# Kernel optimization log

Hardware: AMD Instinct MI355X
Metric: run time of the kernel (lower is better)

Reference implementation:

```python
import jax, jax.numpy as jnp
import numpy as np


def setup_inputs() -> dict:
    key = jax.random.key(0)
    ks = jax.random.split(key, 10)
    B, L, Din, Dout = 64, 512, 256, 256
    s = 0.05
    inp = jax.random.normal(ks[0], (B, L, Din), jnp.float32)
    ci = jax.random.randint(ks[1], (B, L), 0, L)
    # valid coref indices: ci[:, i] must be in [0, i] (refers to an already-produced state)
    ci = ci % (jnp.arange(L) + 1)[None, :]
    p = lambda k, sh: jax.random.normal(k, sh, jnp.float32) * s
    return {
        "inp": inp,
        "last_coref_idx": ci,
        "Wr": p(ks[2], (Din, Dout)), "br": jnp.zeros((Dout,), jnp.float32),
        "Ur": p(ks[3], (Dout, Dout)),
        "Wz": p(ks[4], (Din, Dout)), "bz": jnp.zeros((Dout,), jnp.float32),
        "Uz": p(ks[5], (Dout, Dout)),
        "Wh": p(ks[6], (Din, Dout)), "bh": jnp.zeros((Dout,), jnp.float32),
        "Uh": p(ks[7], (Dout, Dout)),
        "k1": p(ks[8], (Din, 1)),
        "k2": p(ks[9], (Din, 1)),
    }


def reference(inp, last_coref_idx, Wr, br, Ur, Wz, bz, Uz, Wh, bh, Uh, k1, k2):
    B, L, Din = inp.shape
    Dout = Wr.shape[1]
    split = Dout // 2
    bidx = jnp.arange(B)

    def step(carry, xs):
        h_last, hist = carry            # h_last [B,Dout], hist [L,B,Dout]
        x, c, i = xs                    # x [B,Din], c [B] int, i scalar step index
        # coref = state_history[c-1][b] if c > 0 else zeros
        coref = hist[jnp.clip(c - 1, 0), bidx]
        coref = jnp.where((c > 0)[:, None], coref, jnp.zeros_like(coref))
        # attention between h_last-half and coref-half
        e = jnp.concatenate([x @ k1, x @ k2], axis=1)      # [B,2]
        a = jax.nn.softmax(e, axis=1)[:, 0:1]              # [B,1]
        mt = jnp.concatenate([a * h_last[:, :split], (1.0 - a) * coref[:, split:]], axis=1)
        r = jax.nn.sigmoid(x @ Wr + br + mt @ Ur)
        z = jax.nn.sigmoid(x @ Wz + bz + mt @ Uz)
        h_ = jnp.tanh(x @ Wh + bh + r * (mt @ Uh))
        h = (1.0 - z) * mt + z * h_
        hist = jax.lax.dynamic_update_index_in_dim(hist, h, i, 0)
        return (h, hist), h

    h0 = jnp.zeros((B, Dout), inp.dtype)
    hist0 = jnp.zeros((L, B, Dout), inp.dtype)
    xs = (jnp.swapaxes(inp, 0, 1), jnp.swapaxes(last_coref_idx, 0, 1), jnp.arange(L))
    _, ys = jax.lax.scan(step, (h0, hist0), xs)            # ys [L,B,Dout]
    return jnp.swapaxes(ys, 0, 1)                          # [B,L,Dout]
```

## Files before the change

### kernel.cpp

```cpp
#include <hip/hip_runtime.h>
#include <stdint.h>
#include <stddef.h>

typedef _Float16 half_t;
typedef _Float16 half2_t __attribute__((ext_vector_type(2)));
typedef _Float16 half8_t __attribute__((ext_vector_type(8)));
typedef float    floatx4 __attribute__((ext_vector_type(4)));
typedef uint32_t u32x4   __attribute__((ext_vector_type(4)));
typedef int      intx4   __attribute__((ext_vector_type(4)));

#define SEQ_L 512
#define NBATCH 64
#define DIM 256
#define NTOT (NBATCH * SEQ_L)

__device__ __forceinline__ int dot4i8(uint32_t a, uint32_t b, int c) {
#if defined(__has_builtin)
#if __has_builtin(__builtin_amdgcn_sdot4)
  return __builtin_amdgcn_sdot4((int)a, (int)b, c, false);
#else
  int s = c;
  s += (int)(int8_t)(a)       * (int)(int8_t)(b);
  s += (int)(int8_t)(a >> 8)  * (int)(int8_t)(b >> 8);
  s += (int)(int8_t)(a >> 16) * (int)(int8_t)(b >> 16);
  s += (int)(int8_t)(a >> 24) * (int)(int8_t)(b >> 24);
  return s;
#endif
#else
  int s = c;
  s += (int)(int8_t)(a)       * (int)(int8_t)(b);
  s += (int)(int8_t)(a >> 8)  * (int)(int8_t)(b >> 8);
  s += (int)(int8_t)(a >> 16) * (int)(int8_t)(b >> 16);
  s += (int)(int8_t)(a >> 24) * (int)(int8_t)(b >> 24);
  return s;
#endif
}

__device__ __forceinline__ float sigmoidf_fast(float x) {
  return 1.0f / (1.0f + __expf(-x));
}
__device__ __forceinline__ float tanhf_fast(float x) {
  float e = __expf(2.0f * x);
  return 1.0f - 2.0f / (e + 1.0f);
}

__global__ void conv_w_kernel(const float* __restrict__ Wr,
                              const float* __restrict__ Wz,
                              const float* __restrict__ Wh,
                              half_t* __restrict__ Wt) {
  int n = blockIdx.x;
  int k = threadIdx.x;
  const float* W = (n < 256) ? Wr : ((n < 512) ? Wz : Wh);
  int j = n & 255;
  Wt[(size_t)n * DIM + k] = (half_t)W[(size_t)k * DIM + j];
}

__global__ __launch_bounds__(256) void attn_a_kernel(const float* __restrict__ inp,
                                                     const float* __restrict__ k1,
                                                     const float* __restrict__ k2,
                                                     float* __restrict__ a_arr) {
  int row  = blockIdx.x * 4 + (threadIdx.x >> 6);
  int lane = threadIdx.x & 63;
  const float4* x4 = (const float4*)(inp + (size_t)row * DIM);
  float4 xv  = x4[lane];
  float4 k1v = ((const float4*)k1)[lane];
  float4 k2v = ((const float4*)k2)[lane];
  float e1 = xv.x * k1v.x + xv.y * k1v.y + xv.z * k1v.z + xv.w * k1v.w;
  float e2 = xv.x * k2v.x + xv.y * k2v.y + xv.z * k2v.z + xv.w * k2v.w;
#pragma unroll
  for (int off = 32; off >= 1; off >>= 1) {
    e1 += __shfl_xor(e1, off);
    e2 += __shfl_xor(e2, off);
  }
  if (lane == 0) a_arr[row] = 1.0f / (1.0f + __expf(e2 - e1));
}

__global__ __launch_bounds__(256) void uscale_kernel(const float* __restrict__ Ur,
                                                     const float* __restrict__ Uz,
                                                     const float* __restrict__ Uh,
                                                     float* __restrict__ su) {
  const int g = blockIdx.x;
  const int j = threadIdx.x;
  const float* U = (g == 0) ? Ur : ((g == 1) ? Uz : Uh);
  float m = 0.0f;
  for (int k = 0; k < DIM; ++k) m = fmaxf(m, fabsf(U[(size_t)k * DIM + j]));
  su[g * DIM + j] = fmaxf(m, 1e-30f) * (1.0f / 127.0f);
}

__global__ __launch_bounds__(256) void upack_kernel(const float* __restrict__ Ur,
                                                    const float* __restrict__ Uz,
                                                    const float* __restrict__ Uh,
                                                    const float* __restrict__ su,
                                                    uint32_t* __restrict__ Ui8) {
  const int g = blockIdx.x;
  const int j = threadIdx.x;
  const float* U = (g == 0) ? Ur : ((g == 1) ? Uz : Uh);
  const float r = 1.0f / su[g * DIM + j];
  for (int q = 0; q < 64; ++q) {
    uint32_t w = 0;
#pragma unroll
    for (int t = 0; t < 4; ++t) {
      float v = U[(size_t)(q * 4 + t) * DIM + j] * r;
      int mi = __float2int_rn(v);
      mi = mi < -127 ? -127 : (mi > 127 ? 127 : mi);
      w |= ((uint32_t)(mi & 0xFF)) << (8 * t);
    }
    Ui8[((size_t)g * 64 + q) * DIM + j] = w;
  }
}

__global__ __launch_bounds__(256) void gemm_p_kernel(const float* __restrict__ X,
                                                     const half_t* __restrict__ Wt,
                                                     half_t* __restrict__ P) {
  __shared__ __align__(16) half_t As[128][32];
  __shared__ __align__(16) half_t Bs[128][32];
  const int tid  = threadIdx.x;
  const int bm   = blockIdx.x * 128;
  const int bn   = blockIdx.y * 128;
  const int lane = tid & 63;
  const int wave = tid >> 6;
  const int wm   = (wave >> 1) * 64;
  const int wn   = (wave & 1) * 64;
  const int quad = lane >> 4;
  const int l15  = lane & 15;
  const int r0   = tid >> 2;
  const int kc   = (tid & 3) * 8;

  floatx4 acc[4][4] = {};

  for (int k0 = 0; k0 < DIM; k0 += 32) {
#pragma unroll
    for (int hh = 0; hh < 2; ++hh) {
      int r = r0 + hh * 64;
      const float* asrc = X + (size_t)(bm + r) * DIM + k0 + kc;
      float4 f0 = *(const float4*)(asrc);
      float4 f1 = *(const float4*)(asrc + 4);
      half8_t av;
      av[0] = (half_t)f0.x; av[1] = (half_t)f0.y; av[2] = (half_t)f0.z; av[3] = (half_t)f0.w;
      av[4] = (half_t)f1.x; av[5] = (half_t)f1.y; av[6] = (half_t)f1.z; av[7] = (half_t)f1.w;
      *(half8_t*)(&As[r][kc]) = av;
      *(half8_t*)(&Bs[r][kc]) = *(const half8_t*)(Wt + (size_t)(bn + r) * DIM + k0 + kc);
    }
    __syncthreads();
    half8_t af[4], bf[4];
#pragma unroll
    for (int mi = 0; mi < 4; ++mi)
      af[mi] = *(const half8_t*)(&As[wm + mi * 16 + l15][quad * 8]);
#pragma unroll
    for (int ni = 0; ni < 4; ++ni)
      bf[ni] = *(const half8_t*)(&Bs[wn + ni * 16 + l15][quad * 8]);
#pragma unroll
    for (int mi = 0; mi < 4; ++mi)
#pragma unroll
      for (int ni = 0; ni < 4; ++ni)
        acc[mi][ni] = __builtin_amdgcn_mfma_f32_16x16x32_f16(af[mi], bf[ni], acc[mi][ni], 0, 0, 0);
    __syncthreads();
  }
#pragma unroll
  for (int mi = 0; mi < 4; ++mi)
#pragma unroll
    for (int ni = 0; ni < 4; ++ni) {
      int col = bn + wn + ni * 16 + l15;
#pragma unroll
      for (int rr = 0; rr < 4; ++rr) {
        int row = bm + wm + mi * 16 + quad * 4 + rr;
        P[(size_t)row * 768 + col] = (half_t)acc[mi][ni][rr];
      }
    }
}

__global__ __launch_bounds__(256, 1) void recur_kernel(
    const half_t* __restrict__ P,
    const float* __restrict__ a_arr,
    const int* __restrict__ cidx,
    const uint32_t* __restrict__ Ui8,
    const float* __restrict__ su,
    const float* __restrict__ br, const float* __restrict__ bz, const float* __restrict__ bh,
    float* __restrict__ out) {
  const int j = threadIdx.x;

  __shared__ __align__(16) half_t   hist[SEQ_L][128];
  __shared__ __align__(16) uint32_t mtb[2][64];

  u32x4 ur8[16], uz8[16], uh8[16];
#pragma unroll
  for (int c8 = 0; c8 < 16; ++c8) {
#pragma unroll
    for (int t = 0; t < 4; ++t) {
      const int quad = c8 * 4 + t;
      ur8[c8][t] = Ui8[((size_t)0 * 64 + quad) * DIM + j];
      uz8[c8][t] = Ui8[((size_t)1 * 64 + quad) * DIM + j];
      uh8[c8][t] = Ui8[((size_t)2 * 64 + quad) * DIM + j];
    }
  }

  const float scr = su[0 * DIM + j] * (1.0f / 127.0f);
  const float scz = su[1 * DIM + j] * (1.0f / 127.0f);
  const float sch = su[2 * DIM + j] * (1.0f / 127.0f);
  const float brj = br[j], bzj = bz[j], bhj = bh[j];

  if (j < 64) mtb[0][j] = 0u;

  float mtj = 0.0f;
  const int base = blockIdx.x * SEQ_L;

  const half_t* prow0 = P + (size_t)base * 768;
  float pr_c = (float)prow0[j];
  float pz_c = (float)prow0[DIM + j];
  float ph_c = (float)prow0[2 * DIM + j];
  float a_n = a_arr[base + 1];
  int   c_n = cidx[base + 1];

  __syncthreads();

  for (int i = 0; i < SEQ_L; ++i) {
#pragma unroll
    for (int g8 = 0; g8 < 2; ++g8) {
      asm volatile("" : "+v"(ur8[g8*8+0]), "+v"(ur8[g8*8+1]), "+v"(ur8[g8*8+2]), "+v"(ur8[g8*8+3]),
                         "+v"(ur8[g8*8+4]), "+v"(ur8[g8*8+5]), "+v"(ur8[g8*8+6]), "+v"(ur8[g8*8+7]));
      asm volatile("" : "+v"(uz8[g8*8+0]), "+v"(uz8[g8*8+1]), "+v"(uz8[g8*8+2]), "+v"(uz8[g8*8+3]),
                         "+v"(uz8[g8*8+4]), "+v"(uz8[g8*8+5]), "+v"(uz8[g8*8+6]), "+v"(uz8[g8*8+7]));
      asm volatile("" : "+v"(uh8[g8*8+0]), "+v"(uh8[g8*8+1]), "+v"(uh8[g8*8+2]), "+v"(uh8[g8*8+3]),
                         "+v"(uh8[g8*8+4]), "+v"(uh8[g8*8+5]), "+v"(uh8[g8*8+6]), "+v"(uh8[g8*8+7]));
    }

    const int  cp    = c_n - 1;
    const bool use_h = (cp == i);
    float corefv = 0.0f;
    if (j >= 128) {
      if (c_n > 0 && !use_h) corefv = (float)hist[cp][j - 128];
    }

    const int ip1 = (i + 1 < SEQ_L) ? (i + 1) : i;
    const half_t* prow = P + (size_t)(base + ip1) * 768;
    float pr_x = (float)prow[j];
    float pz_x = (float)prow[DIM + j];
    float ph_x = (float)prow[2 * DIM + j];
    const int ip2 = (i + 2 < SEQ_L) ? (i + 2) : (SEQ_L - 1);
    const float a_x = a_arr[base + ip2];
    const int   c_x = cidx[base + ip2];

    int ar = 0, az = 0, ah = 0;
    const u32x4* mq = (const u32x4*)(&mtb[i & 1][0]);
#pragma unroll
    for (int c8 = 0; c8 < 16; ++c8) {
      u32x4 m4 = mq[c8];
      ar = dot4i8(m4.x, ur8[c8][0], ar);
      az = dot4i8(m4.x, uz8[c8][0], az);
      ah = dot4i8(m4.x, uh8[c8][0], ah);
      ar = dot4i8(m4.y, ur8[c8][1], ar);
      az = dot4i8(m4.y, uz8[c8][1], az);
      ah = dot4i8(m4.y, uh8[c8][1], ah);
      ar = dot4i8(m4.z, ur8[c8][2], ar);
      az = dot4i8(m4.z, uz8[c8][2], az);
      ah = dot4i8(m4.z, uh8[c8][2], ah);
      ar = dot4i8(m4.w, ur8[c8][3], ar);
      az = dot4i8(m4.w, uz8[c8][3], az);
      ah = dot4i8(m4.w, uh8[c8][3], ah);
    }

    const float fr = (float)ar * scr;
    const float fz = (float)az * scz;
    const float fh = (float)ah * sch;
    const float rg = sigmoidf_fast(pr_c + brj + fr);
    const float zg = sigmoidf_fast(pz_c + bzj + fz);
    const float hb = tanhf_fast(ph_c + bhj + rg * fh);
    const float h  = (1.0f - zg) * mtj + zg * hb;

    out[(size_t)(base + i) * DIM + j] = h;
    if (j >= 128) hist[i][j - 128] = (half_t)h;

    float mtn;
    if (j < 128) {
      mtn = a_n * h;
    } else {
      const float coref = (c_n > 0) ? (use_h ? h : corefv) : 0.0f;
      mtn = (1.0f - a_n) * coref;
    }
    mtj = mtn;

    int mi = __float2int_rn(mtn * 127.0f);
    mi = mi < -127 ? -127 : (mi > 127 ? 127 : mi);
    unsigned v0 = (unsigned)mi & 0xFFu;
    unsigned o1 = (unsigned)__shfl_xor((int)v0, 1) & 0xFFu;
    unsigned pp = (j & 1) ? (o1 | (v0 << 8)) : (v0 | (o1 << 8));
    unsigned o2 = (unsigned)__shfl_xor((int)pp, 2);
    unsigned qd = (j & 2) ? ((o2 & 0xFFFFu) | (pp << 16))
                          : ((pp & 0xFFFFu) | (o2 << 16));
    if ((j & 3) == 0) mtb[(i + 1) & 1][j >> 2] = qd;

    pr_c = pr_x; pz_c = pz_x; ph_c = ph_x;
    a_n = a_x;   c_n = c_x;

    __syncthreads();
  }
}

extern "C" void kernel_launch(void* const* d_in, const int* in_sizes, int n_in,
                              void* d_out, int out_size, void* d_ws, size_t ws_size,
                              hipStream_t stream) {
  const float* inp = (const float*)d_in[0];
  const int*   ci  = (const int*)d_in[1];
  const float* Wr  = (const float*)d_in[2];
  const float* br  = (const float*)d_in[3];
  const float* Ur  = (const float*)d_in[4];
  const float* Wz  = (const float*)d_in[5];
  const float* bz  = (const float*)d_in[6];
  const float* Uz  = (const float*)d_in[7];
  const float* Wh  = (const float*)d_in[8];
  const float* bh  = (const float*)d_in[9];
  const float* Uh  = (const float*)d_in[10];
  const float* k1  = (const float*)d_in[11];
  const float* k2  = (const float*)d_in[12];
  float* out = (float*)d_out;

  char* ws = (char*)d_ws;
  half_t*   Wt    = (half_t*)ws;
  half_t*   P     = (half_t*)(ws + 393216);
  float*    a_arr = (float*)(ws + 393216 + 50331648);
  float*    su    = (float*)(ws + 50855936);
  uint32_t* Ui8   = (uint32_t*)(ws + 50859008);

  conv_w_kernel<<<dim3(768), dim3(256), 0, stream>>>(Wr, Wz, Wh, Wt);
  attn_a_kernel<<<dim3(NTOT / 4), dim3(256), 0, stream>>>(inp, k1, k2, a_arr);
  uscale_kernel<<<dim3(3), dim3(256), 0, stream>>>(Ur, Uz, Uh, su);
  upack_kernel<<<dim3(3), dim3(256), 0, stream>>>(Ur, Uz, Uh, su, Ui8);
  gemm_p_kernel<<<dim3(NTOT / 128, 6), dim3(256), 0, stream>>>(inp, Wt, P);
  recur_kernel<<<dim3(NBATCH), dim3(256), 0, stream>>>(P, a_arr, ci, Ui8, su,
                                                       br, bz, bh, out);
}
```

Before: 665.1 us.

## Stream int8 recurrent weights from cache each step instead of holding in registers

```diff
diff --git a/kernel.cpp b/kernel.cpp
--- a/kernel.cpp
+++ b/kernel.cpp
@@ -91,7 +91,7 @@
                                                     const float* __restrict__ Uz,
                                                     const float* __restrict__ Uh,
                                                     const float* __restrict__ su,
-                                                    uint32_t* __restrict__ Ui8) {
+                                                    uint32_t* __restrict__ Ust) {
   const int g = blockIdx.x;
   const int j = threadIdx.x;
   const float* U = (g == 0) ? Ur : ((g == 1) ? Uz : Uh);
@@ -105,7 +105,8 @@
       mi = mi < -127 ? -127 : (mi > 127 ? 127 : mi);
       w |= ((uint32_t)(mi & 0xFF)) << (8 * t);
     }
-    Ui8[((size_t)g * 64 + q) * DIM + j] = w;
+    const int c = g * 16 + (q >> 2);
+    Ust[((size_t)c * 256 + j) * 4 + (q & 3)] = w;
   }
 }
 
@@ -173,7 +174,7 @@
     const half_t* __restrict__ P,
     const float* __restrict__ a_arr,
     const int* __restrict__ cidx,
-    const uint32_t* __restrict__ Ui8,
+    const uint32_t* __restrict__ Ust,
     const float* __restrict__ su,
     const float* __restrict__ br, const float* __restrict__ bz, const float* __restrict__ bh,
     float* __restrict__ out) {
@@ -182,22 +183,12 @@
   __shared__ __align__(16) half_t   hist[SEQ_L][128];
   __shared__ __align__(16) uint32_t mtb[2][64];
 
-  u32x4 ur8[16], uz8[16], uh8[16];
-#pragma unroll
-  for (int c8 = 0; c8 < 16; ++c8) {
-#pragma unroll
-    for (int t = 0; t < 4; ++t) {
-      const int quad = c8 * 4 + t;
-      ur8[c8][t] = Ui8[((size_t)0 * 64 + quad) * DIM + j];
-      uz8[c8][t] = Ui8[((size_t)1 * 64 + quad) * DIM + j];
-      uh8[c8][t] = Ui8[((size_t)2 * 64 + quad) * DIM + j];
-    }
-  }
-
   const float scr = su[0 * DIM + j] * (1.0f / 127.0f);
   const float scz = su[1 * DIM + j] * (1.0f / 127.0f);
   const float sch = su[2 * DIM + j] * (1.0f / 127.0f);
   const float brj = br[j], bzj = bz[j], bhj = bh[j];
+
+  const u32x4* upv = (const u32x4*)Ust;
 
   if (j < 64) mtb[0][j] = 0u;
 
@@ -214,15 +205,7 @@
   __syncthreads();
 
   for (int i = 0; i < SEQ_L; ++i) {
-#pragma unroll
-    for (int g8 = 0; g8 < 2; ++g8) {
-      asm volatile("" : "+v"(ur8[g8*8+0]), "+v"(ur8[g8*8+1]), "+v"(ur8[g8*8+2]), "+v"(ur8[g8*8+3]),
-                         "+v"(ur8[g8*8+4]), "+v"(ur8[g8*8+5]), "+v"(ur8[g8*8+6]), "+v"(ur8[g8*8+7]));
-      asm volatile("" : "+v"(uz8[g8*8+0]), "+v"(uz8[g8*8+1]), "+v"(uz8[g8*8+2]), "+v"(uz8[g8*8+3]),
-                         "+v"(uz8[g8*8+4]), "+v"(uz8[g8*8+5]), "+v"(uz8[g8*8+6]), "+v"(uz8[g8*8+7]));
-      asm volatile("" : "+v"(uh8[g8*8+0]), "+v"(uh8[g8*8+1]), "+v"(uh8[g8*8+2]), "+v"(uh8[g8*8+3]),
-                         "+v"(uh8[g8*8+4]), "+v"(uh8[g8*8+5]), "+v"(uh8[g8*8+6]), "+v"(uh8[g8*8+7]));
-    }
+    asm volatile("" : "+v"(upv));
 
     const int  cp    = c_n - 1;
     const bool use_h = (cp == i);
@@ -243,20 +226,23 @@
     int ar = 0, az = 0, ah = 0;
     const u32x4* mq = (const u32x4*)(&mtb[i & 1][0]);
 #pragma unroll
-    for (int c8 = 0; c8 < 16; ++c8) {
-      u32x4 m4 = mq[c8];
-      ar = dot4i8(m4.x, ur8[c8][0], ar);
-      az = dot4i8(m4.x, uz8[c8][0], az);
-      ah = dot4i8(m4.x, uh8[c8][0], ah);
-      ar = dot4i8(m4.y, ur8[c8][1], ar);
-      az = dot4i8(m4.y, uz8[c8][1], az);
-      ah = dot4i8(m4.y, uh8[c8][1], ah);
-      ar = dot4i8(m4.z, ur8[c8][2], ar);
-      az = dot4i8(m4.z, uz8[c8][2], az);
-      ah = dot4i8(m4.z, uh8[c8][2], ah);
-      ar = dot4i8(m4.w, ur8[c8][3], ar);
-      az = dot4i8(m4.w, uz8[c8][3], az);
-      ah = dot4i8(m4.w, uh8[c8][3], ah);
+    for (int cq = 0; cq < 16; ++cq) {
+      u32x4 m4 = mq[cq];
+      u32x4 u0 = upv[(0 * 16 + cq) * 256 + j];
+      u32x4 u1 = upv[(1 * 16 + cq) * 256 + j];
+      u32x4 u2 = upv[(2 * 16 + cq) * 256 + j];
+      ar = dot4i8(m4.x, u0[0], ar);
+      ar = dot4i8(m4.y, u0[1], ar);
+      ar = dot4i8(m4.z, u0[2], ar);
+      ar = dot4i8(m4.w, u0[3], ar);
+      az = dot4i8(m4.x, u1[0], az);
+      az = dot4i8(m4.y, u1[1], az);
+      az = dot4i8(m4.z, u1[2], az);
+      az = dot4i8(m4.w, u1[3], az);
+      ah = dot4i8(m4.x, u2[0], ah);
+      ah = dot4i8(m4.y, u2[1], ah);
+      ah = dot4i8(m4.z, u2[2], ah);
+      ah = dot4i8(m4.w, u2[3], ah);
     }
 
     const float fr = (float)ar * scr;
@@ -319,13 +305,13 @@
   half_t*   P     = (half_t*)(ws + 393216);
   float*    a_arr = (float*)(ws + 393216 + 50331648);
   float*    su    = (float*)(ws + 50855936);
-  uint32_t* Ui8   = (uint32_t*)(ws + 50859008);
+  uint32_t* Ust   = (uint32_t*)(ws + 50859008);
 
   conv_w_kernel<<<dim3(768), dim3(256), 0, stream>>>(Wr, Wz, Wh, Wt);
   attn_a_kernel<<<dim3(NTOT / 4), dim3(256), 0, stream>>>(inp, k1, k2, a_arr);
   uscale_kernel<<<dim3(3), dim3(256), 0, stream>>>(Ur, Uz, Uh, su);
-  upack_kernel<<<dim3(3), dim3(256), 0, stream>>>(Ur, Uz, Uh, su, Ui8);
+  upack_kernel<<<dim3(3), dim3(256), 0, stream>>>(Ur, Uz, Uh, su, Ust);
   gemm_p_kernel<<<dim3(NTOT / 128, 6), dim3(256), 0, stream>>>(inp, Wt, P);
-  recur_kernel<<<dim3(NBATCH), dim3(256), 0, stream>>>(P, a_arr, ci, Ui8, su,
+  recur_kernel<<<dim3(NBATCH), dim3(256), 0, stream>>>(P, a_arr, ci, Ust, su,
                                                        br, bz, bh, out);
 }
```

Result: slower. 1.434 ms (+115.6%).
